# Kernel optimization log

Hardware: AMD Instinct MI355X
Metric: run time of the kernel (lower is better)

## Reference

```python
import jax, jax.numpy as jnp
import numpy as np

# --- GridEncoder config (matches torch-ngp defaults) ---
D = 3                 # input_dim
L = 16                # num_levels
C = 2                 # level_dim
H = 16                # base_resolution
PLS = 2.0             # per_level_scale
LOG2_HASHMAP = 19
MAX_PARAMS = 2 ** LOG2_HASHMAP
PRIMES = (1, 2654435761, 805459861)  # fast_hash primes for D=3
ALIGN_CORNERS = False


def _level_meta():
    """Replicates the offsets computation in GridEncoder.__init__ and the
    kernel's per-level resolution / hash-vs-dense decision."""
    metas = []
    off = 0
    for l in range(L):
        res = int(np.ceil(H * PLS ** l))            # kernel: ceil(exp2(l*S)*H - 1) + 1 == H*2^l here
        full = (res if ALIGN_CORNERS else res + 1) ** D
        params = min(MAX_PARAMS, full)
        params = int(np.ceil(params / 8) * 8)       # pad to multiple of 8
        hashed = full > params                      # kernel: stride > hashmap_size after index loop
        metas.append((off, params, res, hashed))
        off += params
    return metas, off

METAS, TOTAL_PARAMS = _level_meta()


def setup_inputs() -> dict:
    key = jax.random.key(0)
    k1, k2 = jax.random.split(key)
    B = 1048576
    inputs = jax.random.uniform(k1, (B, D), dtype=jnp.float32, minval=-1.0, maxval=1.0)
    # reset_parameters(): uniform(-1e-4, 1e-4)
    embeddings = jax.random.uniform(k2, (TOTAL_PARAMS, C), dtype=jnp.float32,
                                    minval=-1e-4, maxval=1e-4)
    return {"inputs": inputs, "embeddings": embeddings}


def _grid_encode(x, embeddings):
    """x: [B, D] in [0, 1]. Returns [B, L*C]."""
    corner_bits = jnp.array([[(c >> d) & 1 for d in range(D)] for c in range(2 ** D)],
                            dtype=jnp.uint32)                       # [8, D]
    primes = jnp.array(PRIMES, dtype=jnp.uint32)
    outs = []
    for l, (off, size, res, hashed) in enumerate(METAS):
        scale = float(np.exp2(l) * H - 1.0)                          # exp2(l*S)*H - 1, S = log2(2) = 1
        pos = x * scale + (0.0 if ALIGN_CORNERS else 0.5)            # [B, D]
        pg_f = jnp.floor(pos)
        frac = pos - pg_f                                            # [B, D] linear interp weights
        pg = pg_f.astype(jnp.uint32)                                 # [B, D]
        corners = pg[None, :, :] + corner_bits[:, None, :]           # [8, B, D]
        # N-linear interpolation weights: prod over dims of frac / (1-frac)
        w = jnp.prod(jnp.where(corner_bits[:, None, :] == 1,
                               frac[None, :, :], 1.0 - frac[None, :, :]), axis=-1)  # [8, B]
        if hashed:
            # fast_hash: xor of pos_grid[d] * primes[d] in wrapping uint32
            idx = corners[..., 0] * primes[0]
            for d in range(1, D):
                idx = idx ^ (corners[..., d] * primes[d])
        else:
            base = res if ALIGN_CORNERS else res + 1
            stride = jnp.array([base ** d for d in range(D)], dtype=jnp.uint32)
            idx = (corners * stride).sum(axis=-1).astype(jnp.uint32)
        idx = (idx % jnp.uint32(size)) + jnp.uint32(off)             # [8, B]
        emb = embeddings[idx]                                        # [8, B, C] gather
        outs.append(jnp.einsum('kb,kbc->bc', w, emb))                # [B, C]
    return jnp.concatenate(outs, axis=-1)                            # [B, L*C], level-major


def reference(inputs, embeddings):
    bound = 1.0
    x = (inputs + bound) / (2.0 * bound)   # map to [0, 1]
    return _grid_encode(x, embeddings)
```

## Files before the change

kernel.cpp:

```cpp
#include <hip/hip_runtime.h>
#include <cstdint>


namespace {

using f32x2 = __attribute__((ext_vector_type(2))) float;
using f32x4 = __attribute__((ext_vector_type(4))) float;

__device__ __forceinline__ void level_setup(
    float x, float y, float z, uint32_t l,
    uint32_t idx[8], float w[8]) {
  uint32_t res = 16u << l;
  float scale = (float)res - 1.0f;

  float px = x * scale + 0.5f;
  float py = y * scale + 0.5f;
  float pz = z * scale + 0.5f;
  float gx = floorf(px), gy = floorf(py), gz = floorf(pz);
  float rx = px - gx, ry = py - gy, rz = pz - gz;
  uint32_t ix = (uint32_t)gx, iy = (uint32_t)gy, iz = (uint32_t)gz;

  uint32_t off = (l >= 3u) ? (l * 524288u - 1257368u)
                           : ((l == 0u) ? 0u : ((l == 1u) ? 4920u : 40864u));
  bool hashed = (l >= 3u);

  uint32_t base = res + 1u;
  uint32_t bb = base * base;
  const uint32_t P2 = 2654435761u, P3 = 805459861u;

  uint32_t dy0 = iy * base, dy1 = dy0 + base;
  uint32_t dz0 = iz * bb,   dz1 = dz0 + bb;
  uint32_t hy0 = iy * P2,   hy1 = hy0 + P2;
  uint32_t hz0 = iz * P3,   hz1 = hz0 + P3;

#pragma unroll
  for (int c = 0; c < 8; ++c) {
    uint32_t cx = ix + (uint32_t)(c & 1);
    uint32_t h = (cx ^ ((c & 2) ? hy1 : hy0) ^ ((c & 4) ? hz1 : hz0)) & 0x7FFFFu;
    uint32_t d = cx + ((c & 2) ? dy1 : dy0) + ((c & 4) ? dz1 : dz0);
    idx[c] = (hashed ? h : d) + off;
  }

  float wx1 = rx, wx0 = 1.0f - rx;
  float wy1 = ry, wy0 = 1.0f - ry;
  float wz1 = rz, wz0 = 1.0f - rz;
#pragma unroll
  for (int c = 0; c < 8; ++c) {
    w[c] = ((c & 1) ? wx1 : wx0) *
           ((c & 2) ? wy1 : wy0) *
           ((c & 4) ? wz1 : wz0);
  }
}

__global__ __launch_bounds__(256) void gather_lm_kernel(
    const float* __restrict__ in,
    const f32x2* __restrict__ emb,
    f32x2* __restrict__ ws,
    uint32_t B) {
  uint32_t l = blockIdx.y;
  uint32_t p = blockIdx.x * 256u + threadIdx.x;
  if (p >= B) return;

  float x = (__builtin_nontemporal_load(&in[p * 3 + 0]) + 1.0f) * 0.5f;
  float y = (__builtin_nontemporal_load(&in[p * 3 + 1]) + 1.0f) * 0.5f;
  float z = (__builtin_nontemporal_load(&in[p * 3 + 2]) + 1.0f) * 0.5f;

  uint32_t idx[8];
  float w[8];
  level_setup(x, y, z, l, idx, w);

  f32x2 e[8];
#pragma unroll
  for (int c = 0; c < 8; ++c) e[c] = emb[idx[c]];

  float o0 = 0.0f, o1 = 0.0f;
#pragma unroll
  for (int c = 0; c < 8; ++c) {
    o0 = fmaf(w[c], e[c].x, o0);
    o1 = fmaf(w[c], e[c].y, o1);
  }

  f32x2 r; r.x = o0; r.y = o1;
  __builtin_nontemporal_store(r, &ws[(size_t)l * B + p]);
}

__global__ __launch_bounds__(256) void transpose_kernel(
    const f32x2* __restrict__ ws,
    f32x4* __restrict__ out,
    uint32_t B) {
  __shared__ f32x2 lds[16 * 257];
  uint32_t tid = threadIdx.x;
  uint32_t p0 = blockIdx.x * 256u;

#pragma unroll
  for (uint32_t l = 0; l < 16u; ++l) {
    lds[l * 257u + tid] =
        __builtin_nontemporal_load(&ws[(size_t)l * B + p0 + tid]);
  }
  __syncthreads();

#pragma unroll
  for (uint32_t m = 0; m < 8u; ++m) {
    uint32_t lin = m * 256u + tid;
    uint32_t q = lin >> 3;
    uint32_t j2 = lin & 7u;
    f32x2 a = lds[(2u * j2)      * 257u + q];
    f32x2 b = lds[(2u * j2 + 1u) * 257u + q];
    f32x4 v; v.x = a.x; v.y = a.y; v.z = b.x; v.w = b.y;
    __builtin_nontemporal_store(v, &out[(size_t)p0 * 8u + lin]);
  }
}

__global__ __launch_bounds__(256) void grid_encode_fallback(
    const float* __restrict__ in, const f32x2* __restrict__ emb,
    f32x4* __restrict__ out, uint32_t B) {
  uint32_t p = blockIdx.x * 256u + threadIdx.x;
  if (p >= B) return;
  float x = (in[p * 3 + 0] + 1.0f) * 0.5f;
  float y = (in[p * 3 + 1] + 1.0f) * 0.5f;
  float z = (in[p * 3 + 2] + 1.0f) * 0.5f;
#pragma unroll 1
  for (uint32_t l = 0; l < 16u; l += 2u) {
    uint32_t ia[8], ib[8]; float wa[8], wb[8];
    level_setup(x, y, z, l, ia, wa);
    level_setup(x, y, z, l + 1u, ib, wb);
    f32x2 ea[8], eb[8];
#pragma unroll
    for (int c = 0; c < 8; ++c) ea[c] = emb[ia[c]];
#pragma unroll
    for (int c = 0; c < 8; ++c) eb[c] = emb[ib[c]];
    float a0 = 0, a1 = 0, b0 = 0, b1 = 0;
#pragma unroll
    for (int c = 0; c < 8; ++c) {
      a0 = fmaf(wa[c], ea[c].x, a0);
      a1 = fmaf(wa[c], ea[c].y, a1);
      b0 = fmaf(wb[c], eb[c].x, b0);
      b1 = fmaf(wb[c], eb[c].y, b1);
    }
    f32x4 v; v.x = a0; v.y = a1; v.z = b0; v.w = b1;
    out[(size_t)p * 8u + (l >> 1)] = v;
  }
}

}

extern "C" void kernel_launch(void* const* d_in, const int* in_sizes, int n_in,
                              void* d_out, int out_size, void* d_ws, size_t ws_size,
                              hipStream_t stream) {
  (void)n_in; (void)out_size;
  const float* in = (const float*)d_in[0];
  const f32x2* emb = (const f32x2*)d_in[1];
  f32x4* out = (f32x4*)d_out;
  uint32_t B = (uint32_t)(in_sizes[0] / 3);
  uint32_t pblocks = (B + 255u) / 256u;

  size_t ws_needed = (size_t)16 * B * sizeof(f32x2);
  if (ws_size >= ws_needed) {
    f32x2* ws = (f32x2*)d_ws;
    hipLaunchKernelGGL(gather_lm_kernel, dim3(pblocks, 16), dim3(256), 0,
                       stream, in, emb, ws, B);
    hipLaunchKernelGGL(transpose_kernel, dim3(pblocks), dim3(256), 0,
                       stream, ws, out, B);
  } else {
    hipLaunchKernelGGL(grid_encode_fallback, dim3(pblocks), dim3(256), 0,
                       stream, in, emb, out, B);
  }
}
```

Measured before the change: 617.9 us.

## Pair x-adjacent corner gathers into 16-byte loads and batch transpose tiles

The gather path now fetches two x-neighbouring corners with a single 16-byte load when their indices are adjacent and the pair is aligned. For hashed levels adjacency follows from the xor with an even x coordinate, and for dense levels it is checked per pair, with the elements swapped when the index is odd. This cuts the number of scattered load instructions. Separately, the transpose kernel now processes four 256-point tiles per block with a barrier between tiles, and it uses plain loads and stores instead of nontemporal ones. The branchy per-pair logic can diverge within a wave and adds some select instructions.

```diff
diff --git a/kernel.cpp b/kernel.cpp
--- a/kernel.cpp
+++ b/kernel.cpp
@@ -9,7 +9,7 @@
 
 __device__ __forceinline__ void level_setup(
     float x, float y, float z, uint32_t l,
-    uint32_t idx[8], float w[8]) {
+    uint32_t idx[8], float w[8], uint32_t* ix_out, bool* hashed_out) {
   uint32_t res = 16u << l;
   float scale = (float)res - 1.0f;
 
@@ -50,6 +50,29 @@
            ((c & 2) ? wy1 : wy0) *
            ((c & 4) ? wz1 : wz0);
   }
+  *ix_out = ix;
+  *hashed_out = hashed;
+}
+
+__device__ __forceinline__ void gather8(
+    const f32x2* __restrict__ emb, const uint32_t idx[8],
+    uint32_t ix, bool hashed, f32x2 e[8]) {
+  bool ix_even = (ix & 1u) == 0u;
+#pragma unroll
+  for (int c = 0; c < 8; c += 2) {
+    bool ok = hashed ? ix_even : ((idx[c] & 1u) == 0u);
+    if (ok) {
+      f32x4 v = *reinterpret_cast<const f32x4*>(&emb[idx[c] & ~1u]);
+      bool sw = (idx[c] & 1u) != 0u;
+      e[c].x     = sw ? v.z : v.x;
+      e[c].y     = sw ? v.w : v.y;
+      e[c + 1].x = sw ? v.x : v.z;
+      e[c + 1].y = sw ? v.y : v.w;
+    } else {
+      e[c]     = emb[idx[c]];
+      e[c + 1] = emb[idx[c + 1]];
+    }
+  }
 }
 
 __global__ __launch_bounds__(256) void gather_lm_kernel(
@@ -67,11 +90,12 @@
 
   uint32_t idx[8];
   float w[8];
-  level_setup(x, y, z, l, idx, w);
+  uint32_t ix;
+  bool hashed;
+  level_setup(x, y, z, l, idx, w, &ix, &hashed);
 
   f32x2 e[8];
-#pragma unroll
-  for (int c = 0; c < 8; ++c) e[c] = emb[idx[c]];
+  gather8(emb, idx, ix, hashed, e);
 
   float o0 = 0.0f, o1 = 0.0f;
 #pragma unroll
@@ -90,24 +114,28 @@
     uint32_t B) {
   __shared__ f32x2 lds[16 * 257];
   uint32_t tid = threadIdx.x;
-  uint32_t p0 = blockIdx.x * 256u;
+
+  for (uint32_t t = 0; t < 4u; ++t) {
+    uint32_t p0 = (blockIdx.x * 4u + t) * 256u;
+    if (p0 >= B) break;
 
 #pragma unroll
-  for (uint32_t l = 0; l < 16u; ++l) {
-    lds[l * 257u + tid] =
-        __builtin_nontemporal_load(&ws[(size_t)l * B + p0 + tid]);
-  }
-  __syncthreads();
+    for (uint32_t l = 0; l < 16u; ++l) {
+      lds[l * 257u + tid] = ws[(size_t)l * B + p0 + tid];
+    }
+    __syncthreads();
 
 #pragma unroll
-  for (uint32_t m = 0; m < 8u; ++m) {
-    uint32_t lin = m * 256u + tid;
-    uint32_t q = lin >> 3;
-    uint32_t j2 = lin & 7u;
-    f32x2 a = lds[(2u * j2)      * 257u + q];
-    f32x2 b = lds[(2u * j2 + 1u) * 257u + q];
-    f32x4 v; v.x = a.x; v.y = a.y; v.z = b.x; v.w = b.y;
-    __builtin_nontemporal_store(v, &out[(size_t)p0 * 8u + lin]);
+    for (uint32_t m = 0; m < 8u; ++m) {
+      uint32_t lin = m * 256u + tid;
+      uint32_t q = lin >> 3;
+      uint32_t j2 = lin & 7u;
+      f32x2 a = lds[(2u * j2)      * 257u + q];
+      f32x2 b = lds[(2u * j2 + 1u) * 257u + q];
+      f32x4 v; v.x = a.x; v.y = a.y; v.z = b.x; v.w = b.y;
+      out[(size_t)p0 * 8u + lin] = v;
+    }
+    __syncthreads();
   }
 }
 
@@ -122,13 +150,12 @@
 #pragma unroll 1
   for (uint32_t l = 0; l < 16u; l += 2u) {
     uint32_t ia[8], ib[8]; float wa[8], wb[8];
-    level_setup(x, y, z, l, ia, wa);
-    level_setup(x, y, z, l + 1u, ib, wb);
+    uint32_t ixa, ixb; bool ha, hb;
+    level_setup(x, y, z, l, ia, wa, &ixa, &ha);
+    level_setup(x, y, z, l + 1u, ib, wb, &ixb, &hb);
     f32x2 ea[8], eb[8];
-#pragma unroll
-    for (int c = 0; c < 8; ++c) ea[c] = emb[ia[c]];
-#pragma unroll
-    for (int c = 0; c < 8; ++c) eb[c] = emb[ib[c]];
+    gather8(emb, ia, ixa, ha, ea);
+    gather8(emb, ib, ixb, hb, eb);
     float a0 = 0, a1 = 0, b0 = 0, b1 = 0;
 #pragma unroll
     for (int c = 0; c < 8; ++c) {
@@ -159,7 +186,8 @@
     f32x2* ws = (f32x2*)d_ws;
     hipLaunchKernelGGL(gather_lm_kernel, dim3(pblocks, 16), dim3(256), 0,
                        stream, in, emb, ws, B);
-    hipLaunchKernelGGL(transpose_kernel, dim3(pblocks), dim3(256), 0,
+    uint32_t tblocks = (pblocks + 3u) / 4u;
+    hipLaunchKernelGGL(transpose_kernel, dim3(tblocks), dim3(256), 0,
                        stream, ws, out, B);
   } else {
     hipLaunchKernelGGL(grid_encode_fallback, dim3(pblocks), dim3(256), 0,
```

New measurement: 656.6 us. 6.3% more time.
